# Kernel optimization log

Hardware: AMD Instinct MI355X
Metric: run time of the kernel (lower is better)

The kernel has to match this reference:

```python
import jax, jax.numpy as jnp
import numpy as np

EPS = 1e-8
THRESHOLD = 0.5  # ternary quantization threshold

IN_FEATURES = 4096
OUT_FEATURES = 4096


def setup_inputs() -> dict:
    key = jax.random.key(0)
    k_x, k_w, k_b = jax.random.split(key, 3)
    x = jax.random.normal(k_x, (2, 2048, IN_FEATURES), dtype=jnp.float32)
    # xavier_uniform init for weight (out, in)
    limit = float(np.sqrt(6.0 / (IN_FEATURES + OUT_FEATURES)))
    weight = jax.random.uniform(k_w, (OUT_FEATURES, IN_FEATURES), dtype=jnp.float32,
                                minval=-limit, maxval=limit)
    bias = jnp.zeros((OUT_FEATURES,), dtype=jnp.float32)
    return {"x": x, "weight": weight, "bias": bias}


def ternary_quantize(w):
    # scale = mean(|w|), clamped; quantize to {-1,0,1} with 0.5 threshold
    scale = jnp.maximum(jnp.mean(jnp.abs(w)), EPS)
    w_norm = w / scale
    q = jnp.sign(w_norm) * (jnp.abs(w_norm) > THRESHOLD).astype(w.dtype)
    return q, scale


def reference(x, weight, bias):
    # eval-mode forward of BitNetLinear (ternary mode, activation scaling on)
    qw, scale = ternary_quantize(weight)
    input_scale = jnp.maximum(jnp.mean(jnp.abs(x)), EPS)
    scaled_x = x / input_scale
    # F.linear: y = x @ W^T + b, with dequantized weight qw*scale
    out = jnp.einsum('bsi,oi->bso', scaled_x, qw * scale) + bias
    return out * input_scale
```

## Files before the change

kernel.cpp:

```cpp
#include <hip/hip_runtime.h>
#include <hip/hip_bf16.h>

#define AS1 __attribute__((address_space(1)))
#define AS3 __attribute__((address_space(3)))

typedef __attribute__((ext_vector_type(8))) short bfrag8;
typedef __attribute__((ext_vector_type(4))) float floatx4;

static constexpr int M = 4096, N = 4096, K = 4096;
static constexpr long long NELEM = 16777216LL;
static constexpr long long N4 = NELEM / 4;
static constexpr int RB = 2048;

__device__ __forceinline__ unsigned short f2bf(float f) {
    unsigned int u = __float_as_uint(f);
    u += 0x7FFFu + ((u >> 16) & 1u);
    return (unsigned short)(u >> 16);
}

__device__ __forceinline__ double block_reduce(double s) {
    #pragma unroll
    for (int off = 32; off > 0; off >>= 1) s += __shfl_down(s, off, 64);
    __shared__ double part[4];
    int lane = threadIdx.x & 63, wv = threadIdx.x >> 6;
    if (lane == 0) part[wv] = s;
    __syncthreads();
    return part[0] + part[1] + part[2] + part[3];
}

__global__ __launch_bounds__(256) void prep_reduce(
        const float* __restrict__ x, unsigned short* __restrict__ xb,
        const float* __restrict__ w,
        double* __restrict__ px, double* __restrict__ pw) {
    const int b = blockIdx.x;
    const bool isW = b >= RB;
    const int rb = isW ? b - RB : b;
    const long long base = (long long)rb * 256 + threadIdx.x;
    const long long S = (long long)RB * 256;

    const float4* src = (const float4*)(isW ? w : x);
    float4 v[8];
    #pragma unroll
    for (int i = 0; i < 8; i++) v[i] = src[base + i * S];

    double s = 0.0;
    #pragma unroll
    for (int i = 0; i < 8; i++) {
        s += (double)fabsf(v[i].x); s += (double)fabsf(v[i].y);
        s += (double)fabsf(v[i].z); s += (double)fabsf(v[i].w);
    }

    if (!isW) {
        ushort4* xb4 = (ushort4*)xb;
        #pragma unroll
        for (int i = 0; i < 8; i++) {
            ushort4 r;
            r.x = f2bf(v[i].x); r.y = f2bf(v[i].y);
            r.z = f2bf(v[i].z); r.w = f2bf(v[i].w);
            xb4[base + i * S] = r;
        }
    }

    double bs = block_reduce(s);
    if (threadIdx.x == 0) (isW ? pw : px)[rb] = bs;
}

__global__ void finalize_scales(const double* __restrict__ px,
                                const double* __restrict__ pw,
                                float* __restrict__ scales) {
    int t = threadIdx.x;
    double sx = 0.0, sw = 0.0;
    #pragma unroll
    for (int i = 0; i < 8; i++) { sx += px[t + i * 256]; sw += pw[t + i * 256]; }
    #pragma unroll
    for (int off = 32; off > 0; off >>= 1) {
        sx += __shfl_down(sx, off, 64);
        sw += __shfl_down(sw, off, 64);
    }
    __shared__ double ax[4], aw[4];
    int lane = t & 63, wv = t >> 6;
    if (lane == 0) { ax[wv] = sx; aw[wv] = sw; }
    __syncthreads();
    if (t == 0) {
        double fsx = ax[0] + ax[1] + ax[2] + ax[3];
        double fsw = aw[0] + aw[1] + aw[2] + aw[3];
        scales[0] = (float)fmax(fsw / (double)NELEM, 1e-8);
        scales[1] = (float)fmax(fsx / (double)NELEM, 1e-8);
    }
}

__device__ __forceinline__ unsigned short tq(float v, float scale_f) {
    float wn = v / scale_f;
    if (fabsf(wn) > 0.5f)
        return (unsigned short)(0x3F80u | ((__float_as_uint(v) >> 16) & 0x8000u));
    return 0;
}

__global__ __launch_bounds__(256) void quantize_w(
        const float* __restrict__ w, unsigned short* __restrict__ qb,
        const float* __restrict__ scales) {
    const float scale_f = scales[0];
    const long long base = (long long)blockIdx.x * 256 + threadIdx.x;
    const long long S = (long long)RB * 256;
    const float4* w4 = (const float4*)w;
    ushort4* q4 = (ushort4*)qb;
    float4 v[8];
    #pragma unroll
    for (int i = 0; i < 8; i++) v[i] = w4[base + i * S];
    #pragma unroll
    for (int i = 0; i < 8; i++) {
        ushort4 r;
        r.x = tq(v[i].x, scale_f); r.y = tq(v[i].y, scale_f);
        r.z = tq(v[i].z, scale_f); r.w = tq(v[i].w, scale_f);
        q4[base + i * S] = r;
    }
}

__global__ __launch_bounds__(256) void gemm_bt(
        const unsigned short* __restrict__ A,
        const unsigned short* __restrict__ B,
        const float* __restrict__ bias,
        const float* __restrict__ scales,
        float* __restrict__ out) {
    __shared__ unsigned short lds[2 * 128 * 64];
    const char* ldsA = (const char*)lds;
    const char* ldsB = (const char*)lds + 16384;

    const int tid = threadIdx.x;
    const int lane = tid & 63;
    const int wv = tid >> 6;
    const int wm = wv & 1;
    const int wn = wv >> 1;
    const int col16 = lane & 15;
    const int quad = lane >> 4;

    const int m0 = blockIdx.y * 128;
    const int n0 = blockIdx.x * 128;

    const int srow = lane >> 3;
    const int scol = ((lane & 7) ^ srow) * 8;

    floatx4 acc[4][4];
    #pragma unroll
    for (int i = 0; i < 4; i++)
        #pragma unroll
        for (int j = 0; j < 4; j++)
            acc[i][j] = (floatx4)0.0f;

    for (int k0 = 0; k0 < K; k0 += 64) {
        #pragma unroll
        for (int j = 0; j < 4; j++) {
            const int c = wv * 4 + j;
            const int row = c * 8 + srow;
            const unsigned short* ga = A + (size_t)(m0 + row) * K + k0 + scol;
            const unsigned short* gb = B + (size_t)(n0 + row) * K + k0 + scol;
            char* la = (char*)lds + c * 1024 + lane * 16;
            char* lb = (char*)lds + 16384 + c * 1024 + lane * 16;
            __builtin_amdgcn_global_load_lds((const AS1 void*)ga, (AS3 void*)la, 16, 0, 0);
            __builtin_amdgcn_global_load_lds((const AS1 void*)gb, (AS3 void*)lb, 16, 0, 0);
        }
        __syncthreads();

        #pragma unroll
        for (int kk = 0; kk < 64; kk += 32) {
            const int kc = (kk >> 3) + quad;
            const int sw = (kc ^ (col16 & 7)) << 4;
            bfrag8 af[4], bfr[4];
            #pragma unroll
            for (int i = 0; i < 4; i++) {
                const int ra = wm * 64 + i * 16 + col16;
                const int rb = wn * 64 + i * 16 + col16;
                af[i]  = *(const bfrag8*)(ldsA + ra * 128 + sw);
                bfr[i] = *(const bfrag8*)(ldsB + rb * 128 + sw);
            }
            #pragma unroll
            for (int i = 0; i < 4; i++)
                #pragma unroll
                for (int j = 0; j < 4; j++)
                    acc[i][j] = __builtin_amdgcn_mfma_f32_16x16x32_bf16(af[i], bfr[j], acc[i][j], 0, 0, 0);
        }
        __syncthreads();
    }

    const float wscale = scales[0];
    const float iscale = scales[1];

    float bv[4];
    #pragma unroll
    for (int j = 0; j < 4; j++)
        bv[j] = bias[n0 + wn * 64 + j * 16 + col16] * iscale;

    #pragma unroll
    for (int i = 0; i < 4; i++) {
        const int mbase = m0 + wm * 64 + i * 16 + quad * 4;
        #pragma unroll
        for (int j = 0; j < 4; j++) {
            const int n = n0 + wn * 64 + j * 16 + col16;
            #pragma unroll
            for (int r = 0; r < 4; r++)
                out[(size_t)(mbase + r) * N + n] = acc[i][j][r] * wscale + bv[j];
        }
    }
}

extern "C" void kernel_launch(void* const* d_in, const int* in_sizes, int n_in,
                              void* d_out, int out_size, void* d_ws, size_t ws_size,
                              hipStream_t stream) {
    const float* x    = (const float*)d_in[0];
    const float* w    = (const float*)d_in[1];
    const float* bias = (const float*)d_in[2];
    float* out = (float*)d_out;

    char* ws = (char*)d_ws;
    float* scales = (float*)ws;
    unsigned short* xb = (unsigned short*)(ws + 16384);
    unsigned short* qb = (unsigned short*)(ws + 16384 + (size_t)NELEM * 2);
    double* px = (double*)qb;
    double* pw = px + RB;

    prep_reduce<<<2 * RB, 256, 0, stream>>>(x, xb, w, px, pw);
    finalize_scales<<<1, 256, 0, stream>>>(px, pw, scales);
    quantize_w<<<RB, 256, 0, stream>>>(w, qb, scales);

    dim3 grid(N / 128, M / 128);
    gemm_bt<<<grid, 256, 0, stream>>>(xb, qb, bias, scales, out);
}
```

Before: 333.3 us.

## Fuse reduction, scale finalize and weight quantize into one cooperative kernel

Replaces the three preprocessing kernels (abs-sum plus bf16 cast, scale finalize, ternary quantize) with a single cooperative-launch kernel of 512 blocks that uses a grid-wide sync between the reduction and the quantization phases. This removes two kernel launches and their gaps, and each block re-reads the weights it just summed, which may hit in cache. In exchange it runs with fewer blocks, so less latency hiding, and depends on all 512 blocks being co-resident for the grid sync. It also moves the partial-sum buffers to a separate workspace region.

```diff
diff --git a/kernel.cpp b/kernel.cpp
--- a/kernel.cpp
+++ b/kernel.cpp
@@ -1,5 +1,8 @@
 #include <hip/hip_runtime.h>
 #include <hip/hip_bf16.h>
+#include <hip/hip_cooperative_groups.h>
+
+namespace cg = cooperative_groups;
 
 #define AS1 __attribute__((address_space(1)))
 #define AS3 __attribute__((address_space(3)))
@@ -9,84 +12,12 @@
 
 static constexpr int M = 4096, N = 4096, K = 4096;
 static constexpr long long NELEM = 16777216LL;
-static constexpr long long N4 = NELEM / 4;
-static constexpr int RB = 2048;
+static constexpr int CB = 512;
 
 __device__ __forceinline__ unsigned short f2bf(float f) {
     unsigned int u = __float_as_uint(f);
     u += 0x7FFFu + ((u >> 16) & 1u);
     return (unsigned short)(u >> 16);
-}
-
-__device__ __forceinline__ double block_reduce(double s) {
-    #pragma unroll
-    for (int off = 32; off > 0; off >>= 1) s += __shfl_down(s, off, 64);
-    __shared__ double part[4];
-    int lane = threadIdx.x & 63, wv = threadIdx.x >> 6;
-    if (lane == 0) part[wv] = s;
-    __syncthreads();
-    return part[0] + part[1] + part[2] + part[3];
-}
-
-__global__ __launch_bounds__(256) void prep_reduce(
-        const float* __restrict__ x, unsigned short* __restrict__ xb,
-        const float* __restrict__ w,
-        double* __restrict__ px, double* __restrict__ pw) {
-    const int b = blockIdx.x;
-    const bool isW = b >= RB;
-    const int rb = isW ? b - RB : b;
-    const long long base = (long long)rb * 256 + threadIdx.x;
-    const long long S = (long long)RB * 256;
-
-    const float4* src = (const float4*)(isW ? w : x);
-    float4 v[8];
-    #pragma unroll
-    for (int i = 0; i < 8; i++) v[i] = src[base + i * S];
-
-    double s = 0.0;
-    #pragma unroll
-    for (int i = 0; i < 8; i++) {
-        s += (double)fabsf(v[i].x); s += (double)fabsf(v[i].y);
-        s += (double)fabsf(v[i].z); s += (double)fabsf(v[i].w);
-    }
-
-    if (!isW) {
-        ushort4* xb4 = (ushort4*)xb;
-        #pragma unroll
-        for (int i = 0; i < 8; i++) {
-            ushort4 r;
-            r.x = f2bf(v[i].x); r.y = f2bf(v[i].y);
-            r.z = f2bf(v[i].z); r.w = f2bf(v[i].w);
-            xb4[base + i * S] = r;
-        }
-    }
-
-    double bs = block_reduce(s);
-    if (threadIdx.x == 0) (isW ? pw : px)[rb] = bs;
-}
-
-__global__ void finalize_scales(const double* __restrict__ px,
-                                const double* __restrict__ pw,
-                                float* __restrict__ scales) {
-    int t = threadIdx.x;
-    double sx = 0.0, sw = 0.0;
-    #pragma unroll
-    for (int i = 0; i < 8; i++) { sx += px[t + i * 256]; sw += pw[t + i * 256]; }
-    #pragma unroll
-    for (int off = 32; off > 0; off >>= 1) {
-        sx += __shfl_down(sx, off, 64);
-        sw += __shfl_down(sw, off, 64);
-    }
-    __shared__ double ax[4], aw[4];
-    int lane = t & 63, wv = t >> 6;
-    if (lane == 0) { ax[wv] = sx; aw[wv] = sw; }
-    __syncthreads();
-    if (t == 0) {
-        double fsx = ax[0] + ax[1] + ax[2] + ax[3];
-        double fsw = aw[0] + aw[1] + aw[2] + aw[3];
-        scales[0] = (float)fmax(fsw / (double)NELEM, 1e-8);
-        scales[1] = (float)fmax(fsx / (double)NELEM, 1e-8);
-    }
 }
 
 __device__ __forceinline__ unsigned short tq(float v, float scale_f) {
@@ -96,23 +27,91 @@
     return 0;
 }
 
-__global__ __launch_bounds__(256) void quantize_w(
+__device__ __forceinline__ void block_reduce2(double& a, double& b) {
+    #pragma unroll
+    for (int off = 32; off > 0; off >>= 1) {
+        a += __shfl_down(a, off, 64);
+        b += __shfl_down(b, off, 64);
+    }
+    __shared__ double pa[4], pb[4];
+    int lane = threadIdx.x & 63, wv = threadIdx.x >> 6;
+    __syncthreads();
+    if (lane == 0) { pa[wv] = a; pb[wv] = b; }
+    __syncthreads();
+    a = pa[0] + pa[1] + pa[2] + pa[3];
+    b = pb[0] + pb[1] + pb[2] + pb[3];
+}
+
+__global__ __launch_bounds__(256, 2) void prep_coop(
+        const float* __restrict__ x, unsigned short* __restrict__ xb,
         const float* __restrict__ w, unsigned short* __restrict__ qb,
-        const float* __restrict__ scales) {
-    const float scale_f = scales[0];
-    const long long base = (long long)blockIdx.x * 256 + threadIdx.x;
-    const long long S = (long long)RB * 256;
+        double* __restrict__ px, double* __restrict__ pw,
+        float* __restrict__ scales) {
+    cg::grid_group grid = cg::this_grid();
+    const long long t = (long long)blockIdx.x * 256 + threadIdx.x;
+    const long long T = (long long)CB * 256;
+
+    const float4* x4 = (const float4*)x;
     const float4* w4 = (const float4*)w;
+    ushort4* xb4 = (ushort4*)xb;
+
+    double sx = 0.0, sw = 0.0;
+    #pragma unroll
+    for (int c = 0; c < 4; c++) {
+        float4 v[8];
+        #pragma unroll
+        for (int i = 0; i < 8; i++) v[i] = x4[t + (c * 8 + i) * T];
+        #pragma unroll
+        for (int i = 0; i < 8; i++) {
+            sx += (double)fabsf(v[i].x); sx += (double)fabsf(v[i].y);
+            sx += (double)fabsf(v[i].z); sx += (double)fabsf(v[i].w);
+        }
+        #pragma unroll
+        for (int i = 0; i < 8; i++) {
+            ushort4 r;
+            r.x = f2bf(v[i].x); r.y = f2bf(v[i].y);
+            r.z = f2bf(v[i].z); r.w = f2bf(v[i].w);
+            xb4[t + (c * 8 + i) * T] = r;
+        }
+    }
+    #pragma unroll
+    for (int c = 0; c < 4; c++) {
+        float4 v[8];
+        #pragma unroll
+        for (int i = 0; i < 8; i++) v[i] = w4[t + (c * 8 + i) * T];
+        #pragma unroll
+        for (int i = 0; i < 8; i++) {
+            sw += (double)fabsf(v[i].x); sw += (double)fabsf(v[i].y);
+            sw += (double)fabsf(v[i].z); sw += (double)fabsf(v[i].w);
+        }
+    }
+    block_reduce2(sx, sw);
+    if (threadIdx.x == 0) { px[blockIdx.x] = sx; pw[blockIdx.x] = sw; }
+    __threadfence();
+    grid.sync();
+
+    double fx = px[threadIdx.x] + px[threadIdx.x + 256];
+    double fw = pw[threadIdx.x] + pw[threadIdx.x + 256];
+    block_reduce2(fx, fw);
+    const float scale_w = (float)fmax(fw / (double)NELEM, 1e-8);
+    const float scale_x = (float)fmax(fx / (double)NELEM, 1e-8);
+    if (blockIdx.x == 0 && threadIdx.x == 0) {
+        scales[0] = scale_w; scales[1] = scale_x;
+    }
+
     ushort4* q4 = (ushort4*)qb;
-    float4 v[8];
-    #pragma unroll
-    for (int i = 0; i < 8; i++) v[i] = w4[base + i * S];
-    #pragma unroll
-    for (int i = 0; i < 8; i++) {
-        ushort4 r;
-        r.x = tq(v[i].x, scale_f); r.y = tq(v[i].y, scale_f);
-        r.z = tq(v[i].z, scale_f); r.w = tq(v[i].w, scale_f);
-        q4[base + i * S] = r;
+    #pragma unroll
+    for (int c = 0; c < 4; c++) {
+        float4 v[8];
+        #pragma unroll
+        for (int i = 0; i < 8; i++) v[i] = w4[t + (c * 8 + i) * T];
+        #pragma unroll
+        for (int i = 0; i < 8; i++) {
+            ushort4 r;
+            r.x = tq(v[i].x, scale_w); r.y = tq(v[i].y, scale_w);
+            r.z = tq(v[i].z, scale_w); r.w = tq(v[i].w, scale_w);
+            q4[t + (c * 8 + i) * T] = r;
+        }
     }
 }
 
@@ -212,15 +211,21 @@
     float* out = (float*)d_out;
 
     char* ws = (char*)d_ws;
-    float* scales = (float*)ws;
+    float*  scales = (float*)ws;
+    double* px     = (double*)(ws + 256);
+    double* pw     = (double*)(ws + 256 + CB * 8);
     unsigned short* xb = (unsigned short*)(ws + 16384);
     unsigned short* qb = (unsigned short*)(ws + 16384 + (size_t)NELEM * 2);
-    double* px = (double*)qb;
-    double* pw = px + RB;
-
-    prep_reduce<<<2 * RB, 256, 0, stream>>>(x, xb, w, px, pw);
-    finalize_scales<<<1, 256, 0, stream>>>(px, pw, scales);
-    quantize_w<<<RB, 256, 0, stream>>>(w, qb, scales);
+
+    {
+        const float* ax = x; unsigned short* axb = xb;
+        const float* aw = w; unsigned short* aqb = qb;
+        double* apx = px; double* apw = pw; float* asc = scales;
+        void* args[] = { (void*)&ax, (void*)&axb, (void*)&aw, (void*)&aqb,
+                         (void*)&apx, (void*)&apw, (void*)&asc };
+        hipLaunchCooperativeKernel((const void*)prep_coop, dim3(CB), dim3(256),
+                                   args, 0, stream);
+    }
 
     dim3 grid(N / 128, M / 128);
     gemm_bt<<<grid, 256, 0, stream>>>(xb, qb, bias, scales, out);
```

New measurement: 447.3 us. 1.34x slower.
